# Kernel optimization log

Hardware: AMD Instinct MI355X
Metric: run time of the kernel (lower is better)

## Reference

```python
import jax, jax.numpy as jnp
import numpy as np

H = 32  # hidden_size
NUM_LAYERS = 3
INPUT_SIZE = 64
STD = 0.1


def setup_inputs() -> dict:
    key = jax.random.key(0)
    ks = jax.random.split(key, 2 * NUM_LAYERS + 2)
    inp = {}
    inp["x"] = jax.random.normal(ks[0], (256, 2048, INPUT_SIZE), dtype=jnp.float32)
    in_dim = INPUT_SIZE
    for l in range(NUM_LAYERS):
        inp[f"W_ih{l}"] = STD * jax.random.normal(ks[1 + 2 * l], (4 * H, in_dim), dtype=jnp.float32)
        inp[f"W_hh{l}"] = STD * jax.random.normal(ks[2 + 2 * l], (4 * H, H), dtype=jnp.float32)
        inp[f"b{l}"] = jnp.zeros((4 * H,), dtype=jnp.float32)  # b_ih + b_hh, both init to 0
        in_dim = H
    inp["W_out"] = STD * jax.random.normal(ks[-1], (1, H), dtype=jnp.float32)
    inp["b_out"] = jnp.zeros((1,), dtype=jnp.float32)
    return inp


def _lstm_layer(x, W_ih, W_hh, b):
    # x: [B, T, D_in] -> h_seq: [B, T, H]
    B = x.shape[0]
    # precompute input-to-gate projections for all timesteps (one big GEMM)
    xg = jnp.einsum('btd,gd->btg', x, W_ih) + b          # [B, T, 4H]
    xg = jnp.swapaxes(xg, 0, 1)                           # [T, B, 4H]
    W_hh_T = W_hh.T                                       # [H, 4H]

    def step(carry, xg_t):
        h, c = carry
        g = xg_t + h @ W_hh_T                             # [B, 4H]
        i = jax.nn.sigmoid(g[:, 0 * H:1 * H])
        f = jax.nn.sigmoid(g[:, 1 * H:2 * H])
        gg = jnp.tanh(g[:, 2 * H:3 * H])
        o = jax.nn.sigmoid(g[:, 3 * H:4 * H])
        c = f * c + i * gg
        h = o * jnp.tanh(c)
        return (h, c), h

    h0 = jnp.zeros((B, H), dtype=x.dtype)
    c0 = jnp.zeros((B, H), dtype=x.dtype)
    _, h_seq = jax.lax.scan(step, (h0, c0), xg)           # h_seq: [T, B, H]
    return jnp.swapaxes(h_seq, 0, 1)                      # [B, T, H]


def reference(x, W_ih0, W_hh0, b0, W_ih1, W_hh1, b1, W_ih2, W_hh2, b2, W_out, b_out):
    h = _lstm_layer(x, W_ih0, W_hh0, b0)
    h = _lstm_layer(h, W_ih1, W_hh1, b1)
    h = _lstm_layer(h, W_ih2, W_hh2, b2)
    last = h[:, -1, :]                                    # [B, H]
    return last @ W_out.T + b_out                         # [B, 1]
```

## Files before the change

kernel.cpp:

```cpp
#include <hip/hip_runtime.h>


typedef float v2f __attribute__((ext_vector_type(2)));

constexpr int T_SEQ  = 2048;
constexpr int CH     = 16;
constexpr int NCHUNK = T_SEQ / CH;
constexpr int NPHASE = NCHUNK + 5;

#define GLOAD_LDS16(gsrc, ldst)                                                              \
    __builtin_amdgcn_global_load_lds((const __attribute__((address_space(1))) void*)(gsrc), \
                                     (__attribute__((address_space(3))) void*)(ldst),        \
                                     16, 0, 0)
#define KEEPV(x) asm volatile("" : "+v"(x))

__device__ __forceinline__ float rcp_f(float x) { return __builtin_amdgcn_rcpf(x); }

template<bool RING>
__device__ __forceinline__ void rec_chunk_rl(int l,
    const v2f* __restrict__ xg_in,
    float* __restrict__ ring_out,
    const float (&whA)[32], const float (&whB)[32],
    float (&hs)[32], float& c, float& hreg,
    float mt, float ca, float cb)
{
    v2f xgr[CH];
#pragma unroll
    for (int tt = 0; tt < CH; ++tt) xgr[tt] = xg_in[tt * 64 + l];

#pragma unroll
    for (int tt = 0; tt < CH; ++tt) {
        float aA0 = xgr[tt].x, aA1 = 0.f, aB0 = xgr[tt].y, aB1 = 0.f;
#pragma unroll
        for (int k = 0; k < 32; k += 2) {
            aA0 = fmaf(hs[k],     whA[k],     aA0);
            aB0 = fmaf(hs[k],     whB[k],     aB0);
            aA1 = fmaf(hs[k + 1], whA[k + 1], aA1);
            aB1 = fmaf(hs[k + 1], whB[k + 1], aB1);
        }
        const float ga = aA0 + aA1, gb = aB0 + aB1;

        const float sA = rcp_f(1.0f + __expf(-ga));
        const float eb = __expf(mt * gb);
        const float tb = fmaf(-2.0f, rcp_f(eb + 1.0f), 1.0f);
        const float vB = fmaf(ca, tb, cb);

        const float fv = __shfl_xor(sA, 32);
        const float ov = __shfl_xor(vB, 32);
        const float cn = fmaf(fv, c, sA * vB);
        const float ec = __expf(2.0f * cn);
        const float hn = ov * fmaf(-2.0f, rcp_f(ec + 1.0f), 1.0f);
        c = cn; hreg = hn;

        if constexpr (RING) { if (l < 32) ring_out[tt * 32 + l] = hn; }

        const int hbits = __float_as_int(hn);
#pragma unroll
        for (int k = 0; k < 32; ++k)
            hs[k] = __int_as_float(__builtin_amdgcn_readlane(hbits, k));
    }
}

__device__ __forceinline__ void feed_h_chunk(int l, const float* __restrict__ hr,
    v2f* __restrict__ xg_out, const v2f (&wA)[16], const v2f (&wB)[16],
    float bA, float bB)
{
#pragma unroll
    for (int tt = 0; tt < CH; ++tt) {
        const float4* h4 = reinterpret_cast<const float4*>(hr + tt * 32);
        v2f a0 = {bA, 0.f}, a1 = {0.f, 0.f}, b0 = {bB, 0.f}, b1 = {0.f, 0.f};
#pragma unroll
        for (int i = 0; i < 8; ++i) {
            const float4 v = h4[i];
            const v2f lo = {v.x, v.y}, hi = {v.z, v.w};
            a0 = lo * wA[2*i] + a0;  a1 = hi * wA[2*i+1] + a1;
            b0 = lo * wB[2*i] + b0;  b1 = hi * wB[2*i+1] + b1;
        }
        xg_out[tt * 64 + l] = (v2f){(a0.x + a1.x) + (a0.y + a1.y),
                                    (b0.x + b1.x) + (b0.y + b1.y)};
    }
}

__device__ __forceinline__ void feed0_chunk(int l, const float* __restrict__ xs,
    v2f* __restrict__ xg_out, const v2f (&wA)[32], const v2f (&wB)[32],
    float bA, float bB)
{
#pragma unroll
    for (int tt = 0; tt < CH; ++tt) {
        const float4* xt = reinterpret_cast<const float4*>(xs + tt * 64);
        v2f a0 = {bA, 0.f}, a1 = {0.f, 0.f}, b0 = {bB, 0.f}, b1 = {0.f, 0.f};
#pragma unroll
        for (int i = 0; i < 16; ++i) {
            const float4 v = xt[i];
            const v2f lo = {v.x, v.y}, hi = {v.z, v.w};
            a0 = lo * wA[2*i] + a0;  a1 = hi * wA[2*i+1] + a1;
            b0 = lo * wB[2*i] + b0;  b1 = hi * wB[2*i+1] + b1;
        }
        xg_out[tt * 64 + l] = (v2f){(a0.x + a1.x) + (a0.y + a1.y),
                                    (b0.x + b1.x) + (b0.y + b1.y)};
    }
}

__global__ __launch_bounds__(384, 2)
void lstm3_rl_kernel(const float* __restrict__ x,
    const float* __restrict__ W_ih0, const float* __restrict__ W_hh0, const float* __restrict__ b0,
    const float* __restrict__ W_ih1, const float* __restrict__ W_hh1, const float* __restrict__ b1,
    const float* __restrict__ W_ih2, const float* __restrict__ W_hh2, const float* __restrict__ b2,
    const float* __restrict__ W_out, const float* __restrict__ b_out,
    float* __restrict__ out)
{
    const int bi = blockIdx.x;
    const int w  = threadIdx.x >> 6;
    const int l  = threadIdx.x & 63;

    __shared__ v2f   xg0[2][CH][64];
    __shared__ v2f   xg1[2][CH][64];
    __shared__ v2f   xg2[2][CH][64];
    __shared__ float h0r[2][CH][32];
    __shared__ float h1r[2][CH][32];
    __shared__ float xstage[2][CH * 64];

    if (w == 0) {
        __builtin_amdgcn_s_setprio(1);
        float whA[32], whB[32];
#pragma unroll
        for (int k = 0; k < 32; ++k) {
            whA[k] = W_hh0[l * 32 + k];        KEEPV(whA[k]);
            whB[k] = W_hh0[(l + 64) * 32 + k]; KEEPV(whB[k]);
        }
        const float mt = (l < 32) ? 2.f : 1.f;
        const float ca = (l < 32) ? 1.f : 0.5f;
        const float cb = (l < 32) ? 0.f : 0.5f;
        float hs[32];
#pragma unroll
        for (int k = 0; k < 32; ++k) hs[k] = 0.f;
        float c = 0.f, hreg = 0.f;
        __syncthreads();
        for (int p = 0; p < NPHASE; ++p) {
            const int ci = p - 1;
            if (ci >= 0 && ci < NCHUNK)
                rec_chunk_rl<true>(l, &xg0[ci & 1][0][0], &h0r[ci & 1][0][0],
                                   whA, whB, hs, c, hreg, mt, ca, cb);
            __syncthreads();
        }
    } else if (w == 1) {
        __builtin_amdgcn_s_setprio(1);
        float whA[32], whB[32];
#pragma unroll
        for (int k = 0; k < 32; ++k) {
            whA[k] = W_hh1[l * 32 + k];        KEEPV(whA[k]);
            whB[k] = W_hh1[(l + 64) * 32 + k]; KEEPV(whB[k]);
        }
        const float mt = (l < 32) ? 2.f : 1.f;
        const float ca = (l < 32) ? 1.f : 0.5f;
        const float cb = (l < 32) ? 0.f : 0.5f;
        float hs[32];
#pragma unroll
        for (int k = 0; k < 32; ++k) hs[k] = 0.f;
        float c = 0.f, hreg = 0.f;
        __syncthreads();
        for (int p = 0; p < NPHASE; ++p) {
            const int ci = p - 3;
            if (ci >= 0 && ci < NCHUNK)
                rec_chunk_rl<true>(l, &xg1[ci & 1][0][0], &h1r[ci & 1][0][0],
                                   whA, whB, hs, c, hreg, mt, ca, cb);
            __syncthreads();
        }
    } else if (w == 2) {
        __builtin_amdgcn_s_setprio(1);
        float whA[32], whB[32];
#pragma unroll
        for (int k = 0; k < 32; ++k) {
            whA[k] = W_hh2[l * 32 + k];        KEEPV(whA[k]);
            whB[k] = W_hh2[(l + 64) * 32 + k]; KEEPV(whB[k]);
        }
        const float mt = (l < 32) ? 2.f : 1.f;
        const float ca = (l < 32) ? 1.f : 0.5f;
        const float cb = (l < 32) ? 0.f : 0.5f;
        const float woutv = W_out[l & 31];
        float hs[32];
#pragma unroll
        for (int k = 0; k < 32; ++k) hs[k] = 0.f;
        float c = 0.f, hreg = 0.f;
        __syncthreads();
        for (int p = 0; p < NPHASE; ++p) {
            const int ci = p - 5;
            if (ci >= 0 && ci < NCHUNK)
                rec_chunk_rl<false>(l, &xg2[ci & 1][0][0], nullptr,
                                    whA, whB, hs, c, hreg, mt, ca, cb);
            __syncthreads();
        }
        float s = (l < 32) ? hreg * woutv : 0.f;
#pragma unroll
        for (int off = 16; off; off >>= 1) s += __shfl_xor(s, off);
        if (l == 0) out[bi] = s + b_out[0];
    } else if (w == 3) {
        v2f wA[32], wB[32];
        const v2f* pA = reinterpret_cast<const v2f*>(W_ih0 + l * 64);
        const v2f* pB = reinterpret_cast<const v2f*>(W_ih0 + (l + 64) * 64);
#pragma unroll
        for (int i = 0; i < 32; ++i) { wA[i] = pA[i]; KEEPV(wA[i]); wB[i] = pB[i]; KEEPV(wB[i]); }
        const float bAv = b0[l], bBv = b0[l + 64];
        const float* src = x + (size_t)bi * T_SEQ * 64;
#pragma unroll
        for (int i = 0; i < 4; ++i)
            GLOAD_LDS16(src + i * 256 + l * 4, &xstage[0][i * 256 + l * 4]);
        __syncthreads();
        for (int p = 0; p < NPHASE; ++p) {
            if (p + 1 < NCHUNK) {
                const float* ns = src + (size_t)(p + 1) * CH * 64;
                float* dst = &xstage[(p + 1) & 1][0];
#pragma unroll
                for (int i = 0; i < 4; ++i)
                    GLOAD_LDS16(ns + i * 256 + l * 4, dst + i * 256 + l * 4);
            }
            if (p < NCHUNK)
                feed0_chunk(l, xstage[p & 1], &xg0[p & 1][0][0], wA, wB, bAv, bBv);
            __syncthreads();
        }
    } else if (w == 4) {
        v2f wA[16], wB[16];
        const v2f* pA = reinterpret_cast<const v2f*>(W_ih1 + l * 32);
        const v2f* pB = reinterpret_cast<const v2f*>(W_ih1 + (l + 64) * 32);
#pragma unroll
        for (int i = 0; i < 16; ++i) { wA[i] = pA[i]; KEEPV(wA[i]); wB[i] = pB[i]; KEEPV(wB[i]); }
        const float bAv = b1[l], bBv = b1[l + 64];
        __syncthreads();
        for (int p = 0; p < NPHASE; ++p) {
            const int ci = p - 2;
            if (ci >= 0 && ci < NCHUNK)
                feed_h_chunk(l, &h0r[ci & 1][0][0], &xg1[ci & 1][0][0], wA, wB, bAv, bBv);
            __syncthreads();
        }
    } else {
        v2f wA[16], wB[16];
        const v2f* pA = reinterpret_cast<const v2f*>(W_ih2 + l * 32);
        const v2f* pB = reinterpret_cast<const v2f*>(W_ih2 + (l + 64) * 32);
#pragma unroll
        for (int i = 0; i < 16; ++i) { wA[i] = pA[i]; KEEPV(wA[i]); wB[i] = pB[i]; KEEPV(wB[i]); }
        const float bAv = b2[l], bBv = b2[l + 64];
        __syncthreads();
        for (int p = 0; p < NPHASE; ++p) {
            const int ci = p - 4;
            if (ci >= 0 && ci < NCHUNK)
                feed_h_chunk(l, &h1r[ci & 1][0][0], &xg2[ci & 1][0][0], wA, wB, bAv, bBv);
            __syncthreads();
        }
    }
}

extern "C" void kernel_launch(void* const* d_in, const int* in_sizes, int n_in,
                              void* d_out, int out_size, void* d_ws, size_t ws_size,
                              hipStream_t stream) {
    const float* x      = (const float*)d_in[0];
    const float* W_ih0  = (const float*)d_in[1];
    const float* W_hh0  = (const float*)d_in[2];
    const float* b0     = (const float*)d_in[3];
    const float* W_ih1  = (const float*)d_in[4];
    const float* W_hh1  = (const float*)d_in[5];
    const float* b1     = (const float*)d_in[6];
    const float* W_ih2  = (const float*)d_in[7];
    const float* W_hh2  = (const float*)d_in[8];
    const float* b2     = (const float*)d_in[9];
    const float* W_out  = (const float*)d_in[10];
    const float* b_out  = (const float*)d_in[11];

    lstm3_rl_kernel<<<256, 384, 0, stream>>>(x,
                                             W_ih0, W_hh0, b0,
                                             W_ih1, W_hh1, b1,
                                             W_ih2, W_hh2, b2,
                                             W_out, b_out,
                                             (float*)d_out);
}
```

Measured before the change: 757.6 us.

## Broadcast hidden state through LDS and pad LDS to force one block per CU

The recurrent step no longer broadcasts h with 32 readlane ops per timestep. Each lane now writes its h to a small LDS buffer and then reads it back as float4 vectors feeding packed v2f FMAs, with the recurrent weights held as v2f registers. A dummy 24KB LDS array, touched only by an unreachable branch, is added and launch bounds drop to 1 block per CU so each block gets a CU to itself. The LDS round trip adds latency per step, and the writes and reads within one wave carry no explicit barrier, relying on wave-level execution ordering.

```diff
diff --git a/kernel.cpp b/kernel.cpp
--- a/kernel.cpp
+++ b/kernel.cpp
@@ -17,28 +17,28 @@
 __device__ __forceinline__ float rcp_f(float x) { return __builtin_amdgcn_rcpf(x); }
 
 template<bool RING>
-__device__ __forceinline__ void rec_chunk_rl(int l,
+__device__ __forceinline__ void rec_chunk(int l,
     const v2f* __restrict__ xg_in,
     float* __restrict__ ring_out,
-    const float (&whA)[32], const float (&whB)[32],
-    float (&hs)[32], float& c, float& hreg,
-    float mt, float ca, float cb)
-{
-    v2f xgr[CH];
-#pragma unroll
-    for (int tt = 0; tt < CH; ++tt) xgr[tt] = xg_in[tt * 64 + l];
-
+    float* hbp,
+    const v2f (&whA)[16], const v2f (&whB)[16],
+    float& c, float& hreg, float mt, float ca, float cb)
+{
 #pragma unroll
     for (int tt = 0; tt < CH; ++tt) {
-        float aA0 = xgr[tt].x, aA1 = 0.f, aB0 = xgr[tt].y, aB1 = 0.f;
-#pragma unroll
-        for (int k = 0; k < 32; k += 2) {
-            aA0 = fmaf(hs[k],     whA[k],     aA0);
-            aB0 = fmaf(hs[k],     whB[k],     aB0);
-            aA1 = fmaf(hs[k + 1], whA[k + 1], aA1);
-            aB1 = fmaf(hs[k + 1], whB[k + 1], aB1);
-        }
-        const float ga = aA0 + aA1, gb = aB0 + aB1;
+        const v2f xgv = xg_in[tt * 64 + l];
+        const float4* h4 = reinterpret_cast<const float4*>(hbp);
+        v2f aA0 = {xgv.x, 0.f}, aA1 = {0.f, 0.f};
+        v2f aB0 = {xgv.y, 0.f}, aB1 = {0.f, 0.f};
+#pragma unroll
+        for (int i = 0; i < 8; ++i) {
+            const float4 hv = h4[i];
+            const v2f lo = {hv.x, hv.y}, hi = {hv.z, hv.w};
+            aA0 = lo * whA[2*i]   + aA0;  aA1 = hi * whA[2*i+1] + aA1;
+            aB0 = lo * whB[2*i]   + aB0;  aB1 = hi * whB[2*i+1] + aB1;
+        }
+        const float ga = (aA0.x + aA1.x) + (aA0.y + aA1.y);
+        const float gb = (aB0.x + aB1.x) + (aB0.y + aB1.y);
 
         const float sA = rcp_f(1.0f + __expf(-ga));
         const float eb = __expf(mt * gb);
@@ -52,12 +52,8 @@
         const float hn = ov * fmaf(-2.0f, rcp_f(ec + 1.0f), 1.0f);
         c = cn; hreg = hn;
 
+        hbp[l] = hn;
         if constexpr (RING) { if (l < 32) ring_out[tt * 32 + l] = hn; }
-
-        const int hbits = __float_as_int(hn);
-#pragma unroll
-        for (int k = 0; k < 32; ++k)
-            hs[k] = __int_as_float(__builtin_amdgcn_readlane(hbits, k));
     }
 }
 
@@ -101,8 +97,8 @@
     }
 }
 
-__global__ __launch_bounds__(384, 2)
-void lstm3_rl_kernel(const float* __restrict__ x,
+__global__ __launch_bounds__(384, 1)
+void lstm3_1cu_kernel(const float* __restrict__ x,
     const float* __restrict__ W_ih0, const float* __restrict__ W_hh0, const float* __restrict__ b0,
     const float* __restrict__ W_ih1, const float* __restrict__ W_hh1, const float* __restrict__ b1,
     const float* __restrict__ W_ih2, const float* __restrict__ W_hh2, const float* __restrict__ b2,
@@ -119,75 +115,70 @@
     __shared__ float h0r[2][CH][32];
     __shared__ float h1r[2][CH][32];
     __shared__ float xstage[2][CH * 64];
+    __shared__ float hb[3][64];
+    __shared__ float pad_lds[6144];
+
+    if (bi == 0x7FFFFFFF) { pad_lds[threadIdx.x] = 0.f; out[0] = pad_lds[threadIdx.x ^ 1]; }
 
     if (w == 0) {
         __builtin_amdgcn_s_setprio(1);
-        float whA[32], whB[32];
-#pragma unroll
-        for (int k = 0; k < 32; ++k) {
-            whA[k] = W_hh0[l * 32 + k];        KEEPV(whA[k]);
-            whB[k] = W_hh0[(l + 64) * 32 + k]; KEEPV(whB[k]);
-        }
+        v2f whA[16], whB[16];
+        const v2f* hA = reinterpret_cast<const v2f*>(W_hh0 + l * 32);
+        const v2f* hB = reinterpret_cast<const v2f*>(W_hh0 + (l + 64) * 32);
+#pragma unroll
+        for (int i = 0; i < 16; ++i) { whA[i] = hA[i]; KEEPV(whA[i]); whB[i] = hB[i]; KEEPV(whB[i]); }
         const float mt = (l < 32) ? 2.f : 1.f;
         const float ca = (l < 32) ? 1.f : 0.5f;
         const float cb = (l < 32) ? 0.f : 0.5f;
-        float hs[32];
-#pragma unroll
-        for (int k = 0; k < 32; ++k) hs[k] = 0.f;
+        hb[0][l] = 0.f;
         float c = 0.f, hreg = 0.f;
         __syncthreads();
         for (int p = 0; p < NPHASE; ++p) {
             const int ci = p - 1;
             if (ci >= 0 && ci < NCHUNK)
-                rec_chunk_rl<true>(l, &xg0[ci & 1][0][0], &h0r[ci & 1][0][0],
-                                   whA, whB, hs, c, hreg, mt, ca, cb);
+                rec_chunk<true>(l, &xg0[ci & 1][0][0], &h0r[ci & 1][0][0], hb[0],
+                                whA, whB, c, hreg, mt, ca, cb);
             __syncthreads();
         }
     } else if (w == 1) {
         __builtin_amdgcn_s_setprio(1);
-        float whA[32], whB[32];
-#pragma unroll
-        for (int k = 0; k < 32; ++k) {
-            whA[k] = W_hh1[l * 32 + k];        KEEPV(whA[k]);
-            whB[k] = W_hh1[(l + 64) * 32 + k]; KEEPV(whB[k]);
-        }
+        v2f whA[16], whB[16];
+        const v2f* hA = reinterpret_cast<const v2f*>(W_hh1 + l * 32);
+        const v2f* hB = reinterpret_cast<const v2f*>(W_hh1 + (l + 64) * 32);
+#pragma unroll
+        for (int i = 0; i < 16; ++i) { whA[i] = hA[i]; KEEPV(whA[i]); whB[i] = hB[i]; KEEPV(whB[i]); }
         const float mt = (l < 32) ? 2.f : 1.f;
         const float ca = (l < 32) ? 1.f : 0.5f;
         const float cb = (l < 32) ? 0.f : 0.5f;
-        float hs[32];
-#pragma unroll
-        for (int k = 0; k < 32; ++k) hs[k] = 0.f;
+        hb[1][l] = 0.f;
         float c = 0.f, hreg = 0.f;
         __syncthreads();
         for (int p = 0; p < NPHASE; ++p) {
             const int ci = p - 3;
             if (ci >= 0 && ci < NCHUNK)
-                rec_chunk_rl<true>(l, &xg1[ci & 1][0][0], &h1r[ci & 1][0][0],
-                                   whA, whB, hs, c, hreg, mt, ca, cb);
+                rec_chunk<true>(l, &xg1[ci & 1][0][0], &h1r[ci & 1][0][0], hb[1],
+                                whA, whB, c, hreg, mt, ca, cb);
             __syncthreads();
         }
     } else if (w == 2) {
         __builtin_amdgcn_s_setprio(1);
-        float whA[32], whB[32];
-#pragma unroll
-        for (int k = 0; k < 32; ++k) {
-            whA[k] = W_hh2[l * 32 + k];        KEEPV(whA[k]);
-            whB[k] = W_hh2[(l + 64) * 32 + k]; KEEPV(whB[k]);
-        }
+        v2f whA[16], whB[16];
+        const v2f* hA = reinterpret_cast<const v2f*>(W_hh2 + l * 32);
+        const v2f* hB = reinterpret_cast<const v2f*>(W_hh2 + (l + 64) * 32);
+#pragma unroll
+        for (int i = 0; i < 16; ++i) { whA[i] = hA[i]; KEEPV(whA[i]); whB[i] = hB[i]; KEEPV(whB[i]); }
         const float mt = (l < 32) ? 2.f : 1.f;
         const float ca = (l < 32) ? 1.f : 0.5f;
         const float cb = (l < 32) ? 0.f : 0.5f;
         const float woutv = W_out[l & 31];
-        float hs[32];
-#pragma unroll
-        for (int k = 0; k < 32; ++k) hs[k] = 0.f;
+        hb[2][l] = 0.f;
         float c = 0.f, hreg = 0.f;
         __syncthreads();
         for (int p = 0; p < NPHASE; ++p) {
             const int ci = p - 5;
             if (ci >= 0 && ci < NCHUNK)
-                rec_chunk_rl<false>(l, &xg2[ci & 1][0][0], nullptr,
-                                    whA, whB, hs, c, hreg, mt, ca, cb);
+                rec_chunk<false>(l, &xg2[ci & 1][0][0], nullptr, hb[2],
+                                 whA, whB, c, hreg, mt, ca, cb);
             __syncthreads();
         }
         float s = (l < 32) ? hreg * woutv : 0.f;
@@ -265,10 +256,10 @@
     const float* W_out  = (const float*)d_in[10];
     const float* b_out  = (const float*)d_in[11];
 
-    lstm3_rl_kernel<<<256, 384, 0, stream>>>(x,
-                                             W_ih0, W_hh0, b0,
-                                             W_ih1, W_hh1, b1,
-                                             W_ih2, W_hh2, b2,
-                                             W_out, b_out,
-                                             (float*)d_out);
-}
+    lstm3_1cu_kernel<<<256, 384, 0, stream>>>(x,
+                                              W_ih0, W_hh0, b0,
+                                              W_ih1, W_hh1, b1,
+                                              W_ih2, W_hh2, b2,
+                                              W_out, b_out,
+                                              (float*)d_out);
+}
```

Result: slower. 880.1 us (+16.2%).
